# Optimization experiments

Hardware: AMD Instinct MI355X
Metric: run time of the kernel (lower is better)

Reference implementation:

```python
import jax, jax.numpy as jnp
import numpy as np

N_NODES = 100000
N_EDGES = 600000
D = 128  # input_dim == output_dim (required by index_add into zeros_like(x) + residual)
EPS = 1e-5


def _linear_params(key, d_in, d_out):
    kw, kb = jax.random.split(key)
    bound = 1.0 / np.sqrt(d_in)
    w = jax.random.uniform(kw, (d_in, d_out), minval=-bound, maxval=bound, dtype=jnp.float32)
    b = jax.random.uniform(kb, (d_out,), minval=-bound, maxval=bound, dtype=jnp.float32)
    return w, b


def setup_inputs() -> dict:
    key = jax.random.key(0)
    ks = jax.random.split(key, 6)
    x = jax.random.normal(ks[0], (N_NODES, D), dtype=jnp.float32)
    edge_index = jax.random.randint(ks[1], (2, N_EDGES), 0, N_NODES, dtype=jnp.int32)
    w_m1, b_m1 = _linear_params(ks[2], 2 * D, D)
    w_m2, b_m2 = _linear_params(ks[3], D, D)
    w_u1, b_u1 = _linear_params(ks[4], 2 * D, D)
    w_u2, b_u2 = _linear_params(ks[5], D, D)
    gamma = jnp.ones((D,), dtype=jnp.float32)
    beta = jnp.zeros((D,), dtype=jnp.float32)
    return {
        "x": x, "edge_index": edge_index,
        "w_m1": w_m1, "b_m1": b_m1, "w_m2": w_m2, "b_m2": b_m2,
        "w_u1": w_u1, "b_u1": b_u1, "w_u2": w_u2, "b_u2": b_u2,
        "gamma": gamma, "beta": beta,
    }


def _layernorm(h, gamma, beta):
    mu = jnp.mean(h, axis=-1, keepdims=True)
    var = jnp.mean(jnp.square(h - mu), axis=-1, keepdims=True)
    return (h - mu) * jax.lax.rsqrt(var + EPS) * gamma + beta


def reference(x, edge_index, w_m1, b_m1, w_m2, b_m2, w_u1, b_u1, w_u2, b_u2, gamma, beta):
    row, col = edge_index[0], edge_index[1]
    # message MLP on concat of gathered endpoints: [E, 2D] -> [E, D]
    m_in = jnp.concatenate([x[row], x[col]], axis=-1)
    m = jax.nn.relu(m_in @ w_m1 + b_m1) @ w_m2 + b_m2
    # scatter-add messages to destination nodes (index_add along dim 0 with col)
    agg = jax.ops.segment_sum(m, col, num_segments=x.shape[0])
    # update MLP on [N, 2D] -> [N, D]
    u_in = jnp.concatenate([x, agg], axis=-1)
    h = jax.nn.relu(u_in @ w_u1 + b_u1) @ w_u2 + b_u2
    return _layernorm(h, gamma, beta) + x
```

## Files before the change

kernel.cpp:

```cpp
#include <hip/hip_runtime.h>
#include <hip/hip_bf16.h>
#include <stdint.h>

#define N_NODES 100000
#define N_EDGES 600000
#define D 128
#define EPS 1e-5f
#define SCAN_BS 512

#define PREP_BLOCKS 321
#define HIST_BLOCKS 2344
#define XF_BLOCKS   782

typedef __attribute__((ext_vector_type(8))) short short8;
typedef __attribute__((ext_vector_type(16))) float floatx16;


__device__ __forceinline__ uint32_t pack_bf16_rne(float lo, float hi) {
    uint32_t ul = __builtin_bit_cast(uint32_t, lo);
    uint32_t uh = __builtin_bit_cast(uint32_t, hi);
    ul += 0x7fffu + ((ul >> 16) & 1u);
    uh += 0x7fffu + ((uh >> 16) & 1u);
    return (ul >> 16) | (uh & 0xffff0000u);
}

__device__ __forceinline__ unsigned short f32_to_bf16_rne(float f) {
    uint32_t u = __builtin_bit_cast(uint32_t, f);
    u += 0x7fffu + ((u >> 16) & 1u);
    return (unsigned short)(u >> 16);
}

__device__ __forceinline__ float bflo(uint32_t a) { return __builtin_bit_cast(float, a << 16); }
__device__ __forceinline__ float bfhi(uint32_t a) { return __builtin_bit_cast(float, a & 0xffff0000u); }

__global__ void prep_hist(const float* __restrict__ w_m1, const float* __restrict__ w_u1,
                          const float* __restrict__ w_u2, const float* __restrict__ w_m2,
                          const float* __restrict__ b_m2,
                          unsigned short* __restrict__ wm1f, unsigned short* __restrict__ wu1tf,
                          unsigned short* __restrict__ wu2f, unsigned short* __restrict__ wcf,
                          float* __restrict__ vb,
                          const int* __restrict__ col, int* __restrict__ count) {
    if (blockIdx.x >= PREP_BLOCKS) {
        int e = (blockIdx.x - PREP_BLOCKS) * 256 + threadIdx.x;
        if (e < N_EDGES) atomicAdd(&count[col[e]], 1);
        return;
    }
    int idx = blockIdx.x * 256 + threadIdx.x;
    if (idx < 32768) {
        int j = idx & 7, lane = (idx >> 3) & 63, t = (idx >> 9) & 3, s = idx >> 11;
        int kk = s * 16 + ((lane >> 5) << 3) + j;
        wm1f[idx] = f32_to_bf16_rne(w_m1[kk * 128 + t * 32 + (lane & 31)]);
    } else if (idx < 49152) {
        int ii = idx - 32768;
        int j = ii & 7, lane = (ii >> 3) & 63, t = (ii >> 9) & 3, s = ii >> 11;
        int kk = s * 16 + ((lane >> 5) << 3) + j;
        wu1tf[ii] = f32_to_bf16_rne(w_u1[kk * 128 + t * 32 + (lane & 31)]);
    } else if (idx < 65536) {
        int ii = idx - 49152;
        int j = ii & 7, lane = (ii >> 3) & 63, t = (ii >> 9) & 3, s = ii >> 11;
        int kk = s * 16 + ((lane >> 5) << 3) + j;
        wu2f[ii] = f32_to_bf16_rne(w_u2[kk * 128 + t * 32 + (lane & 31)]);
    } else if (idx < 81920) {
        int ii = idx - 65536;
        int j = ii & 7, lane = (ii >> 3) & 63, t = (ii >> 9) & 3, s = ii >> 11;
        int kk = s * 16 + ((lane >> 5) << 3) + j;
        int nn = t * 32 + (lane & 31);
        float acc = 0.0f;
        for (int q = 0; q < 128; ++q)
            acc += w_m2[kk * 128 + q] * w_u1[(128 + q) * 128 + nn];
        wcf[ii] = f32_to_bf16_rne(acc);
    } else if (idx < 82048) {
        int nn = idx - 81920;
        float acc = 0.0f;
        for (int q = 0; q < 128; ++q)
            acc += b_m2[q] * w_u1[(128 + q) * 128 + nn];
        vb[nn] = acc;
    }
}

__global__ void scan_one(const int* __restrict__ count, int* __restrict__ base,
                         int* __restrict__ cursor, int* __restrict__ gcur) {
    __shared__ int tmp[SCAN_BS];
    __shared__ int bbase;
    int g = blockIdx.x * SCAN_BS + threadIdx.x;
    int v = (g < N_NODES) ? count[g] : 0;
    tmp[threadIdx.x] = v;
    __syncthreads();
    int acc = v;
#pragma unroll
    for (int off = 1; off < SCAN_BS; off <<= 1) {
        int add = (threadIdx.x >= off) ? tmp[threadIdx.x - off] : 0;
        __syncthreads();
        acc += add;
        tmp[threadIdx.x] = acc;
        __syncthreads();
    }
    if (threadIdx.x == SCAN_BS - 1) bbase = atomicAdd(gcur, acc);
    __syncthreads();
    if (g < N_NODES) {
        int b = bbase + acc - v;
        base[g] = b;
        cursor[g] = b;
    }
}

__launch_bounds__(256, 4)
__global__ void xform_scatter(const float* __restrict__ x, const short8* __restrict__ w1f,
                              const float* __restrict__ b1, unsigned short* __restrict__ xtb,
                              const int* __restrict__ row, const int* __restrict__ col,
                              int* __restrict__ cursor, int* __restrict__ srow) {
    if (blockIdx.x >= XF_BLOCKS) {
        int e = (blockIdx.x - XF_BLOCKS) * 256 + threadIdx.x;
        if (e < N_EDGES) {
            int p = atomicAdd(&cursor[col[e]], 1);
            srow[p] = row[e];
        }
        return;
    }

    __shared__ __align__(16) short h1[4][32 * 136];
    const int wave = threadIdx.x >> 6;
    const int lane = threadIdx.x & 63;
    const int l31  = lane & 31;
    const int half = lane >> 5;
    short* hl = h1[wave];

    const int nbase = (blockIdx.x * 4 + wave) * 32;
    const int n = min(nbase + l31, N_NODES - 1);
    const float* px = x + (size_t)n * D + half * 8;

    union { short8 v; uint32_t u[4]; } fa[8];
#pragma unroll
    for (int s = 0; s < 8; ++s) {
        const int off = s * 16;
        float4 a0 = *(const float4*)(px + off);
        float4 a1 = *(const float4*)(px + off + 4);
        fa[s].u[0] = pack_bf16_rne(a0.x, a0.y); fa[s].u[1] = pack_bf16_rne(a0.z, a0.w);
        fa[s].u[2] = pack_bf16_rne(a1.x, a1.y); fa[s].u[3] = pack_bf16_rne(a1.z, a1.w);
    }

#pragma unroll
    for (int p = 0; p < 2; ++p) {
        floatx16 acc[4];
#pragma unroll
        for (int t = 0; t < 4; ++t) acc[t] = (floatx16)0.0f;
#pragma unroll
        for (int s = 0; s < 8; ++s) {
#pragma unroll
            for (int t = 0; t < 4; ++t) {
                short8 wf = w1f[((p * 8 + s) * 4 + t) * 64 + lane];
                acc[t] = __builtin_amdgcn_mfma_f32_32x32x16_bf16(fa[s].v, wf, acc[t], 0, 0, 0);
            }
        }
#pragma unroll
        for (int t = 0; t < 4; ++t) {
            float bias = p ? b1[t * 32 + l31] : 0.0f;
#pragma unroll
            for (int r = 0; r < 16; ++r) {
                int m = (r & 3) + 8 * (r >> 2) + 4 * half;
                hl[m * 136 + t * 32 + l31] = (short)f32_to_bf16_rne(acc[t][r] + bias);
            }
        }
#pragma unroll
        for (int it = 0; it < 8; ++it) {
            int off = it * 512 + lane * 8;
            int r2 = off >> 7;
            int c2 = off & 127;
            if (nbase + r2 < N_NODES) {
                short8 v = *(const short8*)(hl + r2 * 136 + c2);
                *(short8*)(xtb + (size_t)(nbase + r2) * 256 + p * 128 + c2) = v;
            }
        }
    }
}

__launch_bounds__(256, 8)
__global__ void agg_kernel(const uint32_t* __restrict__ xtb32,
                           const int* __restrict__ srow,
                           const int* __restrict__ base, const int* __restrict__ count,
                           uint32_t* __restrict__ hsum) {
    const int node = blockIdx.x * 4 + (threadIdx.x >> 6);
    const int lane = threadIdx.x & 63;
    if (node >= N_NODES) return;

    const int b   = base[node];
    const int deg = count[node];

    const uint32_t xbu = xtb32[(size_t)node * 128 + 64 + lane];
    const float xb_lo = bflo(xbu);
    const float xb_hi = bfhi(xbu);

    float s_lo = 0.0f, s_hi = 0.0f;

    for (int t0 = 0; t0 < deg; t0 += 64) {
        const int nb = min(64, deg - t0);
        int sr = (lane < nb) ? srow[b + t0 + lane] : 0;
        int d = 0;
        for (; d + 4 <= nb; d += 4) {
            int r0 = __shfl(sr, d);
            int r1 = __shfl(sr, d + 1);
            int r2 = __shfl(sr, d + 2);
            int r3 = __shfl(sr, d + 3);
            uint32_t a0 = xtb32[(size_t)r0 * 128 + lane];
            uint32_t a1 = xtb32[(size_t)r1 * 128 + lane];
            uint32_t a2 = xtb32[(size_t)r2 * 128 + lane];
            uint32_t a3 = xtb32[(size_t)r3 * 128 + lane];
            s_lo += fmaxf(bflo(a0) + xb_lo, 0.0f); s_hi += fmaxf(bfhi(a0) + xb_hi, 0.0f);
            s_lo += fmaxf(bflo(a1) + xb_lo, 0.0f); s_hi += fmaxf(bfhi(a1) + xb_hi, 0.0f);
            s_lo += fmaxf(bflo(a2) + xb_lo, 0.0f); s_hi += fmaxf(bfhi(a2) + xb_hi, 0.0f);
            s_lo += fmaxf(bflo(a3) + xb_lo, 0.0f); s_hi += fmaxf(bfhi(a3) + xb_hi, 0.0f);
        }
        if (d + 2 <= nb) {
            int r0 = __shfl(sr, d);
            int r1 = __shfl(sr, d + 1);
            uint32_t a0 = xtb32[(size_t)r0 * 128 + lane];
            uint32_t a1 = xtb32[(size_t)r1 * 128 + lane];
            s_lo += fmaxf(bflo(a0) + xb_lo, 0.0f); s_hi += fmaxf(bfhi(a0) + xb_hi, 0.0f);
            s_lo += fmaxf(bflo(a1) + xb_lo, 0.0f); s_hi += fmaxf(bfhi(a1) + xb_hi, 0.0f);
            d += 2;
        }
        if (d < nb) {
            int r0 = __shfl(sr, d);
            uint32_t a0 = xtb32[(size_t)r0 * 128 + lane];
            s_lo += fmaxf(bflo(a0) + xb_lo, 0.0f); s_hi += fmaxf(bfhi(a0) + xb_hi, 0.0f);
        }
    }
    hsum[(size_t)node * 64 + lane] = pack_bf16_rne(s_lo, s_hi);
}

__launch_bounds__(256, 4)
__global__ void upd_kernel(const float* __restrict__ x, const unsigned short* __restrict__ hsum,
                           const short8* __restrict__ wu1tf, const short8* __restrict__ wcf,
                           const short8* __restrict__ wu2f,
                           const float* __restrict__ b_u1, const float* __restrict__ vb,
                           const int* __restrict__ count,
                           const float* __restrict__ b_u2,
                           const float* __restrict__ gamma, const float* __restrict__ beta,
                           float* __restrict__ out) {
    __shared__ __align__(16) short h1[4][32 * 136];
    const int wave = threadIdx.x >> 6;
    const int lane = threadIdx.x & 63;
    const int l31  = lane & 31;
    const int half = lane >> 5;
    short* hl = h1[wave];

    const int nbase = (blockIdx.x * 4 + wave) * 32;
    const int n = min(nbase + l31, N_NODES - 1);

    const float* px = x + (size_t)n * D + half * 8;
    const unsigned short* ph = hsum + (size_t)n * D + half * 8;

    short8 hfr[8];
#pragma unroll
    for (int s = 0; s < 8; ++s) hfr[s] = *(const short8*)(ph + s * 16);

    float dgv = (float)count[min(nbase + l31, N_NODES - 1)];

    floatx16 acc[4];
#pragma unroll
    for (int t = 0; t < 4; ++t) acc[t] = (floatx16)0.0f;

#pragma unroll
    for (int s = 0; s < 16; ++s) {
        union { short8 v; uint32_t u[4]; } fa;
        const short8* bf;
        if (s < 8) {
            const int off = s * 16;
            float4 a0 = *(const float4*)(px + off);
            float4 a1 = *(const float4*)(px + off + 4);
            fa.u[0] = pack_bf16_rne(a0.x, a0.y); fa.u[1] = pack_bf16_rne(a0.z, a0.w);
            fa.u[2] = pack_bf16_rne(a1.x, a1.y); fa.u[3] = pack_bf16_rne(a1.z, a1.w);
            bf = wu1tf + (s * 4) * 64;
        } else {
            fa.v = hfr[s - 8];
            bf = wcf + ((s - 8) * 4) * 64;
        }
#pragma unroll
        for (int t = 0; t < 4; ++t) {
            short8 wf = bf[t * 64 + lane];
            acc[t] = __builtin_amdgcn_mfma_f32_32x32x16_bf16(fa.v, wf, acc[t], 0, 0, 0);
        }
    }

    float bu1[4], vbt[4];
#pragma unroll
    for (int t = 0; t < 4; ++t) {
        bu1[t] = b_u1[t * 32 + l31];
        vbt[t] = vb[t * 32 + l31];
    }

#pragma unroll
    for (int r = 0; r < 16; ++r) {
        int m = (r & 3) + 8 * (r >> 2) + 4 * half;
        float dg = __shfl(dgv, m, 32);
#pragma unroll
        for (int t = 0; t < 4; ++t) {
            float v = fmaxf(acc[t][r] + bu1[t] + dg * vbt[t], 0.0f);
            hl[m * 136 + t * 32 + l31] = (short)f32_to_bf16_rne(v);
        }
    }

    floatx16 acc2[4];
#pragma unroll
    for (int t = 0; t < 4; ++t) acc2[t] = (floatx16)0.0f;

#pragma unroll
    for (int s = 0; s < 8; ++s) {
        short8 af = *(const short8*)(hl + l31 * 136 + s * 16 + half * 8);
#pragma unroll
        for (int t = 0; t < 4; ++t) {
            short8 wf = wu2f[(s * 4 + t) * 64 + lane];
            acc2[t] = __builtin_amdgcn_mfma_f32_32x32x16_bf16(af, wf, acc2[t], 0, 0, 0);
        }
    }

    float g4[4], be4[4], bias2[4];
#pragma unroll
    for (int t = 0; t < 4; ++t) {
        g4[t]    = gamma[t * 32 + l31];
        be4[t]   = beta[t * 32 + l31];
        bias2[t] = b_u2[t * 32 + l31];
    }

    float* hf = (float*)hl;
#pragma unroll
    for (int p = 0; p < 2; ++p) {
#pragma unroll
        for (int rr = 0; rr < 8; ++rr) {
            int r = p * 8 + rr;
            float hv[4];
            float s1 = 0.0f, s2 = 0.0f;
#pragma unroll
            for (int t = 0; t < 4; ++t) {
                hv[t] = acc2[t][r] + bias2[t];
                s1 += hv[t];
                s2 += hv[t] * hv[t];
            }
#pragma unroll
            for (int mask = 1; mask < 32; mask <<= 1) {
                s1 += __shfl_xor(s1, mask);
                s2 += __shfl_xor(s2, mask);
            }
            float mean = s1 * (1.0f / 128.0f);
            float var  = s2 * (1.0f / 128.0f) - mean * mean;
            float rs   = rsqrtf(var + EPS);
            int m = (r & 3) + 8 * (r >> 2) + 4 * half;
            int mrow = m - 16 * p;
#pragma unroll
            for (int t = 0; t < 4; ++t)
                hf[mrow * 132 + t * 32 + l31] = (hv[t] - mean) * rs * g4[t] + be4[t];
        }
#pragma unroll
        for (int it = 0; it < 8; ++it) {
            int q = it * 64 + lane;
            int r2 = q >> 5;
            int c4 = q & 31;
            int node = nbase + 16 * p + r2;
            if (node < N_NODES) {
                float4 v = *(const float4*)(hf + r2 * 132 + c4 * 4);
                float4 xr = *(const float4*)(x + (size_t)node * D + c4 * 4);
                v.x += xr.x; v.y += xr.y; v.z += xr.z; v.w += xr.w;
                *(float4*)(out + (size_t)node * D + c4 * 4) = v;
            }
        }
    }
}

extern "C" void kernel_launch(void* const* d_in, const int* in_sizes, int n_in,
                              void* d_out, int out_size, void* d_ws, size_t ws_size,
                              hipStream_t stream) {
    const float* x     = (const float*)d_in[0];
    const int*   edge  = (const int*)d_in[1];
    const float* w_m1  = (const float*)d_in[2];
    const float* b_m1  = (const float*)d_in[3];
    const float* w_m2  = (const float*)d_in[4];
    const float* b_m2  = (const float*)d_in[5];
    const float* w_u1  = (const float*)d_in[6];
    const float* b_u1  = (const float*)d_in[7];
    const float* w_u2  = (const float*)d_in[8];
    const float* b_u2  = (const float*)d_in[9];
    const float* gamma = (const float*)d_in[10];
    const float* beta  = (const float*)d_in[11];
    float* out = (float*)d_out;

    char* ws = (char*)d_ws;
    size_t off = 0;
    auto alloc = [&](size_t bytes) { void* p = ws + off; off = (off + bytes + 15) & ~(size_t)15; return p; };

    unsigned short* xtb   = (unsigned short*)alloc((size_t)N_NODES * 256 * 2);
    unsigned short* hsumB = (unsigned short*)alloc((size_t)N_NODES * D * 2);
    unsigned short* wm1f  = (unsigned short*)alloc(256 * 128 * 2);
    unsigned short* wu1tf = (unsigned short*)alloc(128 * 128 * 2);
    unsigned short* wcf   = (unsigned short*)alloc(128 * 128 * 2);
    unsigned short* wu2f  = (unsigned short*)alloc(128 * 128 * 2);
    float* vb    = (float*)alloc(128 * 4);
    int* count   = (int*)alloc((size_t)N_NODES * 4 + 16);
    int* gcur    = count + N_NODES;
    int* base    = (int*)alloc((size_t)N_NODES * 4);
    int* cursor  = (int*)alloc((size_t)N_NODES * 4);
    int* srow    = (int*)alloc((size_t)N_EDGES * 4);

    const int* rowi = edge;
    const int* coli = edge + N_EDGES;
    const int NB = (N_NODES + SCAN_BS - 1) / SCAN_BS;

    (void)hipMemsetAsync(count, 0, (size_t)N_NODES * 4 + 16, stream);

    prep_hist<<<PREP_BLOCKS + HIST_BLOCKS, 256, 0, stream>>>(
        w_m1, w_u1, w_u2, w_m2, b_m2, wm1f, wu1tf, wu2f, wcf, vb, coli, count);

    scan_one<<<NB, SCAN_BS, 0, stream>>>(count, base, cursor, gcur);

    xform_scatter<<<XF_BLOCKS + HIST_BLOCKS, 256, 0, stream>>>(
        x, (const short8*)wm1f, b_m1, xtb, rowi, coli, cursor, srow);

    agg_kernel<<<(N_NODES + 3) / 4, 256, 0, stream>>>(
        (const uint32_t*)xtb, srow, base, count, (uint32_t*)hsumB);
    upd_kernel<<<(N_NODES + 127) / 128, 256, 0, stream>>>(
        x, hsumB, (const short8*)wu1tf, (const short8*)wcf, (const short8*)wu2f,
        b_u1, vb, count, b_u2, gamma, beta, out);
}
```

Measured before the change: 271.1 us.

## Fuse edge aggregation into update kernel via packed node-local indices

Removes the separate aggregation kernel and its bf16 hsum round trip through global memory. Each wave of the update kernel walks the contiguous CSR edge range of its 32 destination nodes and accumulates the ReLU message sums into LDS, which then feed the MFMA update. To find the destination slot per edge, the low 5 bits of the column index are packed into the source-row word. The cost is less parallelism in the gather phase, since one wave now serially walks about 192 edges instead of 4 waves per 4 nodes. It also adds per-edge loads of the destination's transformed features and branchy segment switching.

```diff
diff --git a/kernel.cpp b/kernel.cpp
--- a/kernel.cpp
+++ b/kernel.cpp
@@ -7,6 +7,7 @@
 #define D 128
 #define EPS 1e-5f
 #define SCAN_BS 512
+#define ROW_MASK 0x1FFFF
 
 #define PREP_BLOCKS 321
 #define HIST_BLOCKS 2344
@@ -112,8 +113,9 @@
     if (blockIdx.x >= XF_BLOCKS) {
         int e = (blockIdx.x - XF_BLOCKS) * 256 + threadIdx.x;
         if (e < N_EDGES) {
-            int p = atomicAdd(&cursor[col[e]], 1);
-            srow[p] = row[e];
+            int c = col[e];
+            int p = atomicAdd(&cursor[c], 1);
+            srow[p] = row[e] | ((c & 31) << 17);
         }
         return;
     }
@@ -174,66 +176,13 @@
     }
 }
 
-__launch_bounds__(256, 8)
-__global__ void agg_kernel(const uint32_t* __restrict__ xtb32,
-                           const int* __restrict__ srow,
+__launch_bounds__(256, 4)
+__global__ void upd_kernel(const float* __restrict__ x, const uint32_t* __restrict__ xtb32,
+                           const int* __restrict__ srowpk,
                            const int* __restrict__ base, const int* __restrict__ count,
-                           uint32_t* __restrict__ hsum) {
-    const int node = blockIdx.x * 4 + (threadIdx.x >> 6);
-    const int lane = threadIdx.x & 63;
-    if (node >= N_NODES) return;
-
-    const int b   = base[node];
-    const int deg = count[node];
-
-    const uint32_t xbu = xtb32[(size_t)node * 128 + 64 + lane];
-    const float xb_lo = bflo(xbu);
-    const float xb_hi = bfhi(xbu);
-
-    float s_lo = 0.0f, s_hi = 0.0f;
-
-    for (int t0 = 0; t0 < deg; t0 += 64) {
-        const int nb = min(64, deg - t0);
-        int sr = (lane < nb) ? srow[b + t0 + lane] : 0;
-        int d = 0;
-        for (; d + 4 <= nb; d += 4) {
-            int r0 = __shfl(sr, d);
-            int r1 = __shfl(sr, d + 1);
-            int r2 = __shfl(sr, d + 2);
-            int r3 = __shfl(sr, d + 3);
-            uint32_t a0 = xtb32[(size_t)r0 * 128 + lane];
-            uint32_t a1 = xtb32[(size_t)r1 * 128 + lane];
-            uint32_t a2 = xtb32[(size_t)r2 * 128 + lane];
-            uint32_t a3 = xtb32[(size_t)r3 * 128 + lane];
-            s_lo += fmaxf(bflo(a0) + xb_lo, 0.0f); s_hi += fmaxf(bfhi(a0) + xb_hi, 0.0f);
-            s_lo += fmaxf(bflo(a1) + xb_lo, 0.0f); s_hi += fmaxf(bfhi(a1) + xb_hi, 0.0f);
-            s_lo += fmaxf(bflo(a2) + xb_lo, 0.0f); s_hi += fmaxf(bfhi(a2) + xb_hi, 0.0f);
-            s_lo += fmaxf(bflo(a3) + xb_lo, 0.0f); s_hi += fmaxf(bfhi(a3) + xb_hi, 0.0f);
-        }
-        if (d + 2 <= nb) {
-            int r0 = __shfl(sr, d);
-            int r1 = __shfl(sr, d + 1);
-            uint32_t a0 = xtb32[(size_t)r0 * 128 + lane];
-            uint32_t a1 = xtb32[(size_t)r1 * 128 + lane];
-            s_lo += fmaxf(bflo(a0) + xb_lo, 0.0f); s_hi += fmaxf(bfhi(a0) + xb_hi, 0.0f);
-            s_lo += fmaxf(bflo(a1) + xb_lo, 0.0f); s_hi += fmaxf(bfhi(a1) + xb_hi, 0.0f);
-            d += 2;
-        }
-        if (d < nb) {
-            int r0 = __shfl(sr, d);
-            uint32_t a0 = xtb32[(size_t)r0 * 128 + lane];
-            s_lo += fmaxf(bflo(a0) + xb_lo, 0.0f); s_hi += fmaxf(bfhi(a0) + xb_hi, 0.0f);
-        }
-    }
-    hsum[(size_t)node * 64 + lane] = pack_bf16_rne(s_lo, s_hi);
-}
-
-__launch_bounds__(256, 4)
-__global__ void upd_kernel(const float* __restrict__ x, const unsigned short* __restrict__ hsum,
                            const short8* __restrict__ wu1tf, const short8* __restrict__ wcf,
                            const short8* __restrict__ wu2f,
                            const float* __restrict__ b_u1, const float* __restrict__ vb,
-                           const int* __restrict__ count,
                            const float* __restrict__ b_u2,
                            const float* __restrict__ gamma, const float* __restrict__ beta,
                            float* __restrict__ out) {
@@ -243,18 +192,82 @@
     const int l31  = lane & 31;
     const int half = lane >> 5;
     short* hl = h1[wave];
+    uint32_t* accu = (uint32_t*)hl;
 
     const int nbase = (blockIdx.x * 4 + wave) * 32;
-    const int n = min(nbase + l31, N_NODES - 1);
-
-    const float* px = x + (size_t)n * D + half * 8;
-    const unsigned short* ph = hsum + (size_t)n * D + half * 8;
-
-    short8 hfr[8];
-#pragma unroll
-    for (int s = 0; s < 8; ++s) hfr[s] = *(const short8*)(ph + s * 16);
-
-    float dgv = (float)count[min(nbase + l31, N_NODES - 1)];
+    const int nc = min(nbase + l31, N_NODES - 1);
+
+    const int b_l = base[nc];
+    const int c_l = count[nc];
+    const int ebeg = __shfl(b_l, 0);
+    const int eend = __shfl(b_l, 31) + __shfl(c_l, 31);
+    const float dgv = (float)c_l;
+
+#pragma unroll
+    for (int i = 0; i < 32; ++i) accu[i * 64 + lane] = 0;
+
+    {
+        float s_lo = 0.0f, s_hi = 0.0f;
+        int curnib = -1;
+        for (int t0 = ebeg; t0 < eend; t0 += 64) {
+            const int nb = min(64, eend - t0);
+            int pk = (lane < nb) ? srowpk[t0 + lane] : 0;
+            for (int d = 0; d < nb; d += 4) {
+                int p0 = __shfl(pk, d);
+                int p1 = __shfl(pk, min(d + 1, nb - 1));
+                int p2 = __shfl(pk, min(d + 2, nb - 1));
+                int p3 = __shfl(pk, min(d + 3, nb - 1));
+                int r0 = p0 & ROW_MASK, n0 = p0 >> 17;
+                int r1 = p1 & ROW_MASK, n1 = p1 >> 17;
+                int r2 = p2 & ROW_MASK, n2 = p2 >> 17;
+                int r3 = p3 & ROW_MASK, n3 = p3 >> 17;
+                uint32_t a0 = xtb32[(size_t)r0 * 128 + lane];
+                uint32_t b0 = xtb32[(size_t)(nbase + n0) * 128 + 64 + lane];
+                uint32_t a1 = xtb32[(size_t)r1 * 128 + lane];
+                uint32_t b1v = xtb32[(size_t)(nbase + n1) * 128 + 64 + lane];
+                uint32_t a2 = xtb32[(size_t)r2 * 128 + lane];
+                uint32_t b2v = xtb32[(size_t)(nbase + n2) * 128 + 64 + lane];
+                uint32_t a3 = xtb32[(size_t)r3 * 128 + lane];
+                uint32_t b3v = xtb32[(size_t)(nbase + n3) * 128 + 64 + lane];
+
+                {
+                    float vlo = fmaxf(bflo(a0) + bflo(b0), 0.0f);
+                    float vhi = fmaxf(bfhi(a0) + bfhi(b0), 0.0f);
+                    if (n0 != curnib) {
+                        if (curnib >= 0) accu[curnib * 64 + lane] = pack_bf16_rne(s_lo, s_hi);
+                        curnib = n0; s_lo = vlo; s_hi = vhi;
+                    } else { s_lo += vlo; s_hi += vhi; }
+                }
+                if (d + 1 < nb) {
+                    float vlo = fmaxf(bflo(a1) + bflo(b1v), 0.0f);
+                    float vhi = fmaxf(bfhi(a1) + bfhi(b1v), 0.0f);
+                    if (n1 != curnib) {
+                        accu[curnib * 64 + lane] = pack_bf16_rne(s_lo, s_hi);
+                        curnib = n1; s_lo = vlo; s_hi = vhi;
+                    } else { s_lo += vlo; s_hi += vhi; }
+                }
+                if (d + 2 < nb) {
+                    float vlo = fmaxf(bflo(a2) + bflo(b2v), 0.0f);
+                    float vhi = fmaxf(bfhi(a2) + bfhi(b2v), 0.0f);
+                    if (n2 != curnib) {
+                        accu[curnib * 64 + lane] = pack_bf16_rne(s_lo, s_hi);
+                        curnib = n2; s_lo = vlo; s_hi = vhi;
+                    } else { s_lo += vlo; s_hi += vhi; }
+                }
+                if (d + 3 < nb) {
+                    float vlo = fmaxf(bflo(a3) + bflo(b3v), 0.0f);
+                    float vhi = fmaxf(bfhi(a3) + bfhi(b3v), 0.0f);
+                    if (n3 != curnib) {
+                        accu[curnib * 64 + lane] = pack_bf16_rne(s_lo, s_hi);
+                        curnib = n3; s_lo = vlo; s_hi = vhi;
+                    } else { s_lo += vlo; s_hi += vhi; }
+                }
+            }
+        }
+        if (curnib >= 0) accu[curnib * 64 + lane] = pack_bf16_rne(s_lo, s_hi);
+    }
+
+    const float* px = x + (size_t)nc * D + half * 8;
 
     floatx16 acc[4];
 #pragma unroll
@@ -272,7 +285,7 @@
             fa.u[2] = pack_bf16_rne(a1.x, a1.y); fa.u[3] = pack_bf16_rne(a1.z, a1.w);
             bf = wu1tf + (s * 4) * 64;
         } else {
-            fa.v = hfr[s - 8];
+            fa.v = *(const short8*)((const short*)accu + l31 * 128 + (s - 8) * 16 + half * 8);
             bf = wcf + ((s - 8) * 4) * 64;
         }
 #pragma unroll
@@ -388,7 +401,6 @@
     auto alloc = [&](size_t bytes) { void* p = ws + off; off = (off + bytes + 15) & ~(size_t)15; return p; };
 
     unsigned short* xtb   = (unsigned short*)alloc((size_t)N_NODES * 256 * 2);
-    unsigned short* hsumB = (unsigned short*)alloc((size_t)N_NODES * D * 2);
     unsigned short* wm1f  = (unsigned short*)alloc(256 * 128 * 2);
     unsigned short* wu1tf = (unsigned short*)alloc(128 * 128 * 2);
     unsigned short* wcf   = (unsigned short*)alloc(128 * 128 * 2);
@@ -414,9 +426,8 @@
     xform_scatter<<<XF_BLOCKS + HIST_BLOCKS, 256, 0, stream>>>(
         x, (const short8*)wm1f, b_m1, xtb, rowi, coli, cursor, srow);
 
-    agg_kernel<<<(N_NODES + 3) / 4, 256, 0, stream>>>(
-        (const uint32_t*)xtb, srow, base, count, (uint32_t*)hsumB);
     upd_kernel<<<(N_NODES + 127) / 128, 256, 0, stream>>>(
-        x, hsumB, (const short8*)wu1tf, (const short8*)wcf, (const short8*)wu2f,
-        b_u1, vb, count, b_u2, gamma, beta, out);
-}
+        x, (const uint32_t*)xtb, srow, base, count,
+        (const short8*)wu1tf, (const short8*)wcf, (const short8*)wu2f,
+        b_u1, vb, b_u2, gamma, beta, out);
+}
```

Measured after the change: 269.0 us. Within noise of the previous version (-0.8%).
